# Optimization experiments

Hardware: AMD Instinct MI355X
Metric: run time of the kernel (lower is better)

Reference implementation:

```python
import jax, jax.numpy as jnp
import numpy as np
import math

N, E, D, H, EH, DEPTH = 50000, 800000, 128, 128, 16, 3
RATIO = 0.5
BN_SCALE = 1.0 / math.sqrt(1.0 + 1e-5)  # eval-mode BatchNorm1d: running mean 0, var 1
NEG_SLOPE = 0.01  # leaky_relu default


def setup_inputs() -> dict:
    key = jax.random.key(0)
    ks = jax.random.split(key, 16)
    s = lambda k, shape: jax.random.normal(k, shape, dtype=jnp.float32) * 0.05
    return {
        "x": jax.random.normal(ks[0], (N, D), dtype=jnp.float32),
        "edge_index": jax.random.randint(ks[1], (2, E), 0, N, dtype=jnp.int32),
        "edge_attr": jax.random.uniform(ks[2], (E, EH), dtype=jnp.float32),
        "We_w": s(ks[3], (EH, 1)), "We_b": s(ks[4], (1,)),
        "Wdown": s(ks[5], (DEPTH + 1, H, H)), "bdown": s(ks[6], (DEPTH + 1, H)),
        "Wpool": s(ks[7], (DEPTH, H)),
        "Wup": s(ks[8], (DEPTH, H, H)), "bup": s(ks[9], (DEPTH, H)),
        "gnorm": 1.0 + s(ks[10], (DEPTH + 1, H)), "bnorm": s(ks[11], (DEPTH + 1, H)),
        "Wr": s(ks[12], (D, D)), "br": s(ks[13], (D,)),
        "gr": 1.0 + s(ks[14], (D,)), "brn": s(ks[15], (D,)),
    }


def _bn(x, g, b):
    # eval-mode BatchNorm1d with running_mean=0, running_var=1
    return x * (g * BN_SCALE) + b


def _lrelu(x):
    return jnp.where(x > 0, x, NEG_SLOPE * x)


def _gcn(x, src, dst, w, W, b, fill):
    # PyG GCNConv: add self-loops (fill=1.0, improved -> 2.0), symmetric norm
    n = x.shape[0]
    h = x @ W  # [n, H]
    deg = jax.ops.segment_sum(w, dst, num_segments=n) + fill
    dinv = jax.lax.rsqrt(deg)
    coef = dinv[src] * w * dinv[dst]  # [E]
    agg = jax.ops.segment_sum(coef[:, None] * h[src], dst, num_segments=n)
    return agg + (fill / deg)[:, None] * h + b  # self-loop norm = fill/deg


def _topk_pool(x, src, dst, w, p, k):
    # PyG TopKPooling: score = tanh(x.p/||p||), keep top-k, scale kept x by score,
    # filter edges to kept nodes (masked edges kept at fixed length with weight 0)
    n = x.shape[0]
    score = jnp.tanh((x @ p) / jnp.linalg.norm(p))
    vals, perm = jax.lax.top_k(score, k)
    xp = x[perm] * vals[:, None]
    pos = jnp.full((n,), -1, dtype=jnp.int32).at[perm].set(jnp.arange(k, dtype=jnp.int32))
    ns, nd = pos[src], pos[dst]
    valid = (ns >= 0) & (nd >= 0)
    return (xp, jnp.where(valid, ns, 0), jnp.where(valid, nd, 0),
            jnp.where(valid, w, 0.0), perm)


def reference(x, edge_index, edge_attr, We_w, We_b, Wdown, bdown, Wpool, Wup, bup,
              gnorm, bnorm, Wr, br, gr, brn):
    src, dst = edge_index[0], edge_index[1]
    # edge embedding + min/max normalization
    ew = edge_attr @ We_w[:, 0] + We_b[0]  # [E]
    ew = ew - jnp.min(ew)
    ew = ew / (jnp.max(ew) + 1e-7)
    h = _bn(x, gnorm[0], bnorm[0])
    h = _lrelu(_gcn(h, src, dst, ew, Wdown[0], bdown[0], 1.0))
    xs, es, perms = [h], [(src, dst, ew)], []
    for i in range(DEPTH):
        k = int(math.ceil(RATIO * h.shape[0]))
        h, src, dst, ew, perm = _topk_pool(h, src, dst, ew, Wpool[i], k)
        h = _bn(h, gnorm[i + 1], bnorm[i + 1])
        h = _gcn(h, src, dst, ew, Wdown[i + 1], bdown[i + 1], 1.0)
        if i < DEPTH - 1:
            h = _lrelu(h)
            xs.append(h)
            es.append((src, dst, ew))
        perms.append(perm)
    for i in range(DEPTH):
        j = DEPTH - 1 - i
        res = xs[j]
        src, dst, ew = es[j]
        up = jnp.zeros_like(res).at[perms[j]].set(h)  # scatter unpool
        h = _gcn(res + up, src, dst, ew, Wup[i], bup[i], 2.0)  # improved=True -> fill 2
        if i < DEPTH - 1:
            h = _lrelu(h)
    g = jnp.sum(h, axis=0, keepdims=True)  # global_add_pool, single graph
    g = g @ Wr + br
    return _bn(g, gr, brn)
```

## Files before the change

kernel.cpp:

```cpp
#include <hip/hip_runtime.h>
#include <math.h>

#define N0   50000
#define E0   800000
#define HD   128
#define EHD  16
#define KP1  25000
#define KP2  12500
#define KP3  6250
#define BN_SCALE 0.9999950000374997f
#define NEG_SLOPE 0.01f
#define E1C  400000
#define E2C  120000
#define E3C  40000
#define NBE  782
#define CSB  782

#define NBIN   782
#define EPB    6144
#define NBLK   131
#define NBINP  784

typedef int   vi4 __attribute__((ext_vector_type(4)));
typedef float vf4 __attribute__((ext_vector_type(4)));
typedef __bf16 bfrag8 __attribute__((ext_vector_type(8)));
typedef float  f32x4  __attribute__((ext_vector_type(4)));

__device__ __forceinline__ unsigned fenc(float f) {
    unsigned u = __float_as_uint(f);
    return (u & 0x80000000u) ? ~u : (u | 0x80000000u);
}
__device__ __forceinline__ unsigned packbf2(float a, float b) {
    unsigned ua = __float_as_uint(a);
    unsigned ub = __float_as_uint(b);
    ua = (ua + 0x7FFFu + ((ua >> 16) & 1u)) >> 16;
    ub = (ub + 0x7FFFu + ((ub >> 16) & 1u)) >> 16;
    return ua | (ub << 16);
}
__device__ __forceinline__ void bf8_fma(float* acc, uint4 h, float c) {
    acc[0] += c * __uint_as_float(h.x << 16);
    acc[1] += c * __uint_as_float(h.x & 0xFFFF0000u);
    acc[2] += c * __uint_as_float(h.y << 16);
    acc[3] += c * __uint_as_float(h.y & 0xFFFF0000u);
    acc[4] += c * __uint_as_float(h.z << 16);
    acc[5] += c * __uint_as_float(h.z & 0xFFFF0000u);
    acc[6] += c * __uint_as_float(h.w << 16);
    acc[7] += c * __uint_as_float(h.w & 0xFFFF0000u);
}

__global__ void k_edge_ew(const float* __restrict__ ea, const float* __restrict__ Ww,
                          const float* __restrict__ Wb, float* __restrict__ ew,
                          float2* __restrict__ partials, int E) {
    int e = blockIdx.x * 256 + threadIdx.x;
    float mn = 3.4e38f, mx = -3.4e38f;
    if (e < E) {
        const float4* a4 = (const float4*)(ea + (size_t)e * EHD);
        float s = Wb[0];
        #pragma unroll
        for (int q = 0; q < 4; ++q) {
            float4 a = a4[q];
            s += a.x * Ww[q*4+0] + a.y * Ww[q*4+1] + a.z * Ww[q*4+2] + a.w * Ww[q*4+3];
        }
        ew[e] = s;
        mn = s; mx = s;
    }
    #pragma unroll
    for (int off = 32; off > 0; off >>= 1) {
        mn = fminf(mn, __shfl_xor(mn, off));
        mx = fmaxf(mx, __shfl_xor(mx, off));
    }
    __shared__ float smn[4], smx[4];
    int lane = threadIdx.x & 63, wid = threadIdx.x >> 6;
    if (lane == 0) { smn[wid] = mn; smx[wid] = mx; }
    __syncthreads();
    if (threadIdx.x == 0) {
        float a = fminf(fminf(smn[0], smn[1]), fminf(smn[2], smn[3]));
        float b = fmaxf(fmaxf(smx[0], smx[1]), fmaxf(smx[2], smx[3]));
        partials[blockIdx.x] = make_float2(a, b);
    }
}

__global__ void __launch_bounds__(1024)
k_reduce_mm(const float2* __restrict__ partials, int nb, float* __restrict__ mmv) {
    float mn = 3.4e38f, mx = -3.4e38f;
    for (int i = threadIdx.x; i < nb; i += 1024) {
        float2 t = partials[i];
        mn = fminf(mn, t.x); mx = fmaxf(mx, t.y);
    }
    #pragma unroll
    for (int off = 32; off > 0; off >>= 1) {
        mn = fminf(mn, __shfl_xor(mn, off));
        mx = fmaxf(mx, __shfl_xor(mx, off));
    }
    __shared__ float smn[16], smx[16];
    int lane = threadIdx.x & 63, wid = threadIdx.x >> 6;
    if (lane == 0) { smn[wid] = mn; smx[wid] = mx; }
    __syncthreads();
    if (threadIdx.x == 0) {
        for (int w = 1; w < 16; ++w) { mn = fminf(mn, smn[w]); mx = fmaxf(mx, smx[w]); }
        mmv[0] = mn; mmv[1] = mx;
    }
}

__global__ void __launch_bounds__(1024)
k_ew_sortA(float* __restrict__ ew, const float* __restrict__ mmv,
           const int* __restrict__ src, const int* __restrict__ dst,
           uint2* __restrict__ staging, int* __restrict__ cntM,
           int* __restrict__ locOffM, int E) {
    __shared__ uint2 sEnt[EPB];
    __shared__ int   lhist[NBINP];
    __shared__ int   sOff[NBINP];
    __shared__ int   lcur[NBINP];
    __shared__ int   wtot[16];
    int t = threadIdx.x;
    for (int i = t; i < NBINP; i += 1024) lhist[i] = 0;
    __syncthreads();
    float mn = mmv[0];
    float sc = 1.0f / ((mmv[1] - mn) + 1e-7f);
    int base = blockIdx.x * EPB;
    unsigned entx[6], enty[6];
    int bin6[6];
    #pragma unroll
    for (int it = 0; it < 6; ++it) {
        int e = base + it * 1024 + t;
        bin6[it] = -1;
        if (e < E) {
            float w = (ew[e] - mn) * sc;
            ew[e] = w;
            if (w != 0.0f) {
                int d = dst[e];
                bin6[it] = d >> 6;
                entx[it] = (unsigned)src[e] | ((unsigned)(d & 63) << 16);
                enty[it] = __float_as_uint(w);
                atomicAdd(&lhist[bin6[it]], 1);
            }
        }
    }
    __syncthreads();
    {
        int v = (t < NBINP) ? lhist[t] : 0;
        int lane = t & 63, wid = t >> 6;
        int x = v;
        #pragma unroll
        for (int off = 1; off < 64; off <<= 1) {
            int y = __shfl_up(x, off);
            if (lane >= off) x += y;
        }
        if (lane == 63) wtot[wid] = x;
        __syncthreads();
        int wb = 0;
        for (int w = 0; w < wid; ++w) wb += wtot[w];
        int excl = wb + x - v;
        if (t < NBINP) { sOff[t] = excl; lcur[t] = excl; }
    }
    __syncthreads();
    #pragma unroll
    for (int it = 0; it < 6; ++it) {
        if (bin6[it] >= 0) {
            int slot = atomicAdd(&lcur[bin6[it]], 1);
            sEnt[slot] = make_uint2(entx[it], enty[it]);
        }
    }
    __syncthreads();
    int total = sOff[NBIN];
    uint2* dstS = staging + (size_t)blockIdx.x * EPB;
    for (int i = t; i < total; i += 1024) dstS[i] = sEnt[i];
    int* cRow = cntM + blockIdx.x * NBINP;
    int* oRow = locOffM + blockIdx.x * NBINP;
    for (int i = t; i < NBINP; i += 1024) { cRow[i] = lhist[i]; oRow[i] = sOff[i]; }
}

__global__ void __launch_bounds__(1024)
k_bin_scan2(const int* __restrict__ cntM, int* __restrict__ binBase,
            int* __restrict__ rowptrEnd) {
    int t = threadIdx.x;
    int v = 0;
    if (t < NBIN) {
        for (int blk = 0; blk < NBLK; ++blk) v += cntM[blk * NBINP + t];
    }
    int lane = t & 63, wid = t >> 6;
    int xs = v;
    #pragma unroll
    for (int off = 1; off < 64; off <<= 1) {
        int y = __shfl_up(xs, off);
        if (lane >= off) xs += y;
    }
    __shared__ int wsum[16];
    if (lane == 63) wsum[wid] = xs;
    __syncthreads();
    int wb = 0;
    for (int w = 0; w < wid; ++w) wb += wsum[w];
    int excl = wb + xs - v;
    if (t < NBIN) binBase[t] = excl;
    if (t == NBIN - 1) rowptrEnd[0] = excl + v;
}

__global__ void __launch_bounds__(256)
k_binB2(const int* __restrict__ binBase, const int* __restrict__ cntM,
        const int* __restrict__ locOffM, const uint2* __restrict__ staging,
        int2* __restrict__ csr, float* __restrict__ sumW,
        int* __restrict__ rowptr, int n) {
    __shared__ uint2 raw[2048];
    __shared__ int   lhist[64];
    __shared__ int   lcur[64];
    __shared__ float lw[64];
    __shared__ int2  img[2048];
    __shared__ int   wq[4];
    __shared__ int   totalSh;
    int b = blockIdx.x;
    int t = threadIdx.x;
    int base = binBase[b];
    int c = 0, lo = 0;
    if (t < NBLK) { c = cntM[t * NBINP + b]; lo = locOffM[t * NBINP + b]; }
    int lane = t & 63, wid = t >> 6;
    int x = c;
    #pragma unroll
    for (int off = 1; off < 64; off <<= 1) {
        int y = __shfl_up(x, off);
        if (lane >= off) x += y;
    }
    if (lane == 63) wq[wid] = x;
    if (t < 64) { lhist[t] = 0; lw[t] = 0.f; }
    __syncthreads();
    int wb = 0;
    for (int w = 0; w < wid; ++w) wb += wq[w];
    int pos = wb + x - c;
    if (t == 255) totalSh = wb + x;
    __syncthreads();
    int total = min(totalSh, 2048);
    if (t < NBLK && c > 0) {
        const uint2* st = staging + (size_t)t * EPB + lo;
        for (int j = 0; j < c; ++j) {
            int p = pos + j;
            if (p < 2048) raw[p] = st[j];
        }
    }
    __syncthreads();
    for (int i = t; i < total; i += 256) {
        uint2 en = raw[i];
        int dloc = (en.x >> 16) & 63;
        atomicAdd(&lhist[dloc], 1);
        atomicAdd(&lw[dloc], __uint_as_float(en.y));
    }
    __syncthreads();
    if (t < 64) {
        int cc = lhist[t];
        int xs = cc;
        #pragma unroll
        for (int off = 1; off < 64; off <<= 1) {
            int y = __shfl_up(xs, off);
            if (t >= off) xs += y;
        }
        int excl = xs - cc;
        lcur[t] = excl;
        int v = b * 64 + t;
        if (v < n) { rowptr[v] = base + excl; sumW[v] = lw[t]; }
    }
    __syncthreads();
    for (int i = t; i < total; i += 256) {
        uint2 en = raw[i];
        int dloc = (en.x >> 16) & 63;
        int slot = atomicAdd(&lcur[dloc], 1);
        if (slot < 2048) img[slot] = make_int2((int)(en.x & 0xFFFFu), (int)en.y);
    }
    __syncthreads();
    for (int i = t; i < total; i += 256)
        csr[base + i] = img[i];
}

__global__ void __launch_bounds__(256)
k_wconv(const float* __restrict__ Wsrc, unsigned* __restrict__ WbT) {
    __shared__ ushort Wl[128][136];
    const float* W = Wsrc + (size_t)blockIdx.x * HD * HD;
    unsigned* Wo = WbT + (size_t)blockIdx.x * HD * 64;
    int tid = threadIdx.x;
    #pragma unroll
    for (int it = 0; it < 16; ++it) {
        int idx = it * 256 + tid;
        int k = idx >> 5, c4 = (idx & 31) * 4;
        float4 v = ((const float4*)(W + (size_t)k * HD))[idx & 31];
        Wl[c4 + 0][k] = (ushort)packbf2(v.x, 0.f);
        Wl[c4 + 1][k] = (ushort)packbf2(v.y, 0.f);
        Wl[c4 + 2][k] = (ushort)packbf2(v.z, 0.f);
        Wl[c4 + 3][k] = (ushort)packbf2(v.w, 0.f);
    }
    __syncthreads();
    #pragma unroll
    for (int it = 0; it < 16; ++it) {
        int idx = it * 256 + tid;
        int c = idx >> 5, j = idx & 31;
        uint2 o;
        o.x = (unsigned)Wl[c][4*j + 0] | ((unsigned)Wl[c][4*j + 1] << 16);
        o.y = (unsigned)Wl[c][4*j + 2] | ((unsigned)Wl[c][4*j + 3] << 16);
        ((uint2*)Wo)[c * 32 + j] = o;
    }
}

#define GT_ROWS 64
#define APAD 136
__global__ void __launch_bounds__(256)
k_gemm_mf(const float* __restrict__ A, const unsigned* __restrict__ WbT,
          unsigned* __restrict__ Cb, int n,
          const float* __restrict__ gs, const float* __restrict__ gb,
          const float* __restrict__ up_h, const int* __restrict__ up_pos) {
    __shared__ char ldsb[(64 + 128) * APAD * 2];
    ushort (*Al)[APAD] = (ushort(*)[APAD])ldsb;
    ushort (*Wl)[APAD] = (ushort(*)[APAD])(ldsb + 64 * APAD * 2);
    float  (*outS)[132] = (float(*)[132])ldsb;
    int tid = threadIdx.x;
    int row0 = blockIdx.x * GT_ROWS;
    int maxr = n - row0;
    #pragma unroll
    for (int it = 0; it < 8; ++it) {
        int idx = it * 256 + tid;
        int r = idx >> 5, q = idx & 31;
        float4 v = make_float4(0.f, 0.f, 0.f, 0.f);
        if (r < maxr) {
            v = ((const float4*)(A + (size_t)(row0 + r) * HD))[q];
            if (up_pos) {
                int sl = up_pos[row0 + r];
                if (sl >= 0) {
                    float4 u = ((const float4*)(up_h + (size_t)sl * HD))[q];
                    v.x += u.x; v.y += u.y; v.z += u.z; v.w += u.w;
                }
            }
            if (gs) {
                float4 g4 = ((const float4*)gs)[q];
                float4 b4 = ((const float4*)gb)[q];
                v.x = v.x * (g4.x * BN_SCALE) + b4.x;
                v.y = v.y * (g4.y * BN_SCALE) + b4.y;
                v.z = v.z * (g4.z * BN_SCALE) + b4.z;
                v.w = v.w * (g4.w * BN_SCALE) + b4.w;
            }
        }
        uint2 pk = make_uint2(packbf2(v.x, v.y), packbf2(v.z, v.w));
        *(uint2*)&Al[r][q * 4] = pk;
    }
    #pragma unroll
    for (int it = 0; it < 16; ++it) {
// ... 70 lines not shown
    #pragma unroll
    for (int off = 32; off > 0; off >>= 1) s += __shfl_down(s, off);
    if (lane == 0) ws[wid] = s;
    __syncthreads();
    if (threadIdx.x == 0) {
        __hip_atomic_store(&bsum[blockIdx.x], ws[0] + ws[1] + ws[2] + ws[3],
                           __ATOMIC_RELAXED, __HIP_MEMORY_SCOPE_AGENT);
        unsigned prev = __hip_atomic_fetch_add(dctr, 1u, __ATOMIC_ACQ_REL, __HIP_MEMORY_SCOPE_AGENT);
        lastFlag = (prev == gridDim.x - 1);
    }
    __syncthreads();
    if (!lastFlag) return;
    if (threadIdx.x < 64) {
        int nb = gridDim.x;
        int t = threadIdx.x;
        int v = (t < nb) ? __hip_atomic_load(&bsum[t], __ATOMIC_RELAXED, __HIP_MEMORY_SCOPE_AGENT) : 0;
        int x = v;
        #pragma unroll
        for (int off = 1; off < 64; off <<= 1) {
            int y = __shfl_up(x, off);
            if (t >= off) x += y;
        }
        if (t < nb) bsum[t] = x - v;
        if (t == nb - 1) totalOut[0] = x;
    }
    if (threadIdx.x == 0)
        __hip_atomic_store(dctr, 0u, __ATOMIC_RELAXED, __HIP_MEMORY_SCOPE_AGENT);
}

__global__ void k_chunk_scan(const int* __restrict__ cnt, const int* __restrict__ bo,
                             int* __restrict__ rowptr, int* __restrict__ cursor, int n) {
    __shared__ int wsum[4];
    __shared__ int running;
    int base = blockIdx.x * 1024;
    if (threadIdx.x == 0) running = bo[blockIdx.x];
    __syncthreads();
    int lane = threadIdx.x & 63, wid = threadIdx.x >> 6;
    #pragma unroll
    for (int it = 0; it < 4; ++it) {
        int i = base + it * 256 + threadIdx.x;
        int v = (i < n) ? cnt[i] : 0;
        int x = v;
        #pragma unroll
        for (int off = 1; off < 64; off <<= 1) {
            int y = __shfl_up(x, off);
            if (lane >= off) x += y;
        }
        if (lane == 63) wsum[wid] = x;
        __syncthreads();
        int wb = 0;
        for (int w = 0; w < wid; ++w) wb += wsum[w];
        int excl = running + wb + x - v;
        if (i < n) { rowptr[i] = excl; cursor[i] = excl; }
        __syncthreads();
        if (threadIdx.x == 0) running += wsum[0] + wsum[1] + wsum[2] + wsum[3];
        __syncthreads();
    }
}

__global__ void k_csr_fill(const int* __restrict__ src, const int* __restrict__ dst,
                           const float* __restrict__ w, int* __restrict__ cursor,
                           int2* __restrict__ csr,
                           const int* __restrict__ EinPtr, int EinImm) {
    int Ein = EinPtr ? EinPtr[0] : EinImm;
    int e = blockIdx.x * 256 + threadIdx.x;
    if (e >= Ein) return;
    float wv = w[e];
    if (wv == 0.0f) return;
    int slot = atomicAdd(&cursor[dst[e]], 1);
    csr[slot] = make_int2(src[e], __float_as_int(wv));
}

__global__ void k_deg_dinv(const int* __restrict__ rowptr, const int2* __restrict__ csr,
                           float fill, float* __restrict__ deg, float* __restrict__ dinv, int n) {
    int v = blockIdx.x * 256 + threadIdx.x;
    if (v >= n) return;
    float s = fill;
    int rs = rowptr[v], re = rowptr[v + 1];
    for (int j = rs; j < re; ++j) s += __int_as_float(csr[j].y);
    deg[v] = s;
    dinv[v] = rsqrtf(s);
}

__global__ void k_deg_dinv_d(const float* __restrict__ sumW, float fill,
                             float* __restrict__ deg, float* __restrict__ dinv, int n) {
    int v = blockIdx.x * 256 + threadIdx.x;
    if (v >= n) return;
    float s = fill + sumW[v];
    deg[v] = s;
    dinv[v] = rsqrtf(s);
}

__global__ void __launch_bounds__(256)
k_gcn_gather(const int* __restrict__ rowptr, const int2* __restrict__ csr,
             const float* __restrict__ deg, const float* __restrict__ dinv,
             const unsigned* __restrict__ hWb,
             const float* __restrict__ bias,
             float fill, int n, int lrelu, float* __restrict__ out) {
    int v = blockIdx.x * 4 + (threadIdx.x >> 6);
    int lane = threadIdx.x & 63;
    if (v >= n) return;
    int rs = rowptr[v], re = rowptr[v + 1];
    float dv = dinv[v];
    int quarter = lane >> 4;
    int qi = lane & 15;
    float acc[8];
    #pragma unroll
    for (int i = 0; i < 8; ++i) acc[i] = 0.f;
    for (int base = rs; base < re; base += 64) {
        int idx = base + lane;
        int s_r = 0; float c_r = 0.f;
        if (idx < re) {
            int2 ent = csr[idx];
            s_r = ent.x;
            c_r = dinv[s_r] * __int_as_float(ent.y) * dv;
        }
        int cnt = min(64, re - base);
        int groups = cnt >> 2;
        int t = 0;
        for (; t + 1 < groups; t += 2) {
            int j0 = 4 * t + quarter, j1 = j0 + 4;
            int   s0 = __shfl(s_r, j0); float c0 = __shfl(c_r, j0);
            int   s1 = __shfl(s_r, j1); float c1 = __shfl(c_r, j1);
            uint4 h0 = ((const uint4*)(hWb + (size_t)s0 * 64))[qi];
            uint4 h1 = ((const uint4*)(hWb + (size_t)s1 * 64))[qi];
            bf8_fma(acc, h0, c0);
            bf8_fma(acc, h1, c1);
        }
        for (; t < groups; ++t) {
            int j = 4 * t + quarter;
            int s = __shfl(s_r, j); float c = __shfl(c_r, j);
            uint4 h = ((const uint4*)(hWb + (size_t)s * 64))[qi];
            bf8_fma(acc, h, c);
        }
        int rem = cnt & 3;
        if (quarter < rem) {
            int j = groups * 4 + quarter;
            int s = __shfl(s_r, j); float c = __shfl(c_r, j);
            uint4 h = ((const uint4*)(hWb + (size_t)s * 64))[qi];
            bf8_fma(acc, h, c);
        }
    }
    #pragma unroll
    for (int i = 0; i < 8; ++i) {
        acc[i] += __shfl_xor(acc[i], 16);
        acc[i] += __shfl_xor(acc[i], 32);
    }
    if (quarter == 0) {
        uint4 hs = ((const uint4*)(hWb + (size_t)v * 64))[qi];
        float sc = fill / deg[v];
        float hv[8];
        hv[0] = __uint_as_float(hs.x << 16); hv[1] = __uint_as_float(hs.x & 0xFFFF0000u);
        hv[2] = __uint_as_float(hs.y << 16); hv[3] = __uint_as_float(hs.y & 0xFFFF0000u);
        hv[4] = __uint_as_float(hs.z << 16); hv[5] = __uint_as_float(hs.z & 0xFFFF0000u);
        hv[6] = __uint_as_float(hs.w << 16); hv[7] = __uint_as_float(hs.w & 0xFFFF0000u);
        float4 b0 = ((const float4*)bias)[2 * qi];
        float4 b1 = ((const float4*)bias)[2 * qi + 1];
        float o[8];
        o[0] = acc[0] + sc * hv[0] + b0.x;
        o[1] = acc[1] + sc * hv[1] + b0.y;
        o[2] = acc[2] + sc * hv[2] + b0.z;
        o[3] = acc[3] + sc * hv[3] + b0.w;
        o[4] = acc[4] + sc * hv[4] + b1.x;
        o[5] = acc[5] + sc * hv[5] + b1.y;
        o[6] = acc[6] + sc * hv[6] + b1.z;
        o[7] = acc[7] + sc * hv[7] + b1.w;
        if (lrelu) {
            #pragma unroll
            for (int i = 0; i < 8; ++i) o[i] = (o[i] > 0.f) ? o[i] : NEG_SLOPE * o[i];
        }
        float4* orow = (float4*)(out + (size_t)v * HD);
        orow[2 * qi]     = make_float4(o[0], o[1], o[2], o[3]);
        orow[2 * qi + 1] = make_float4(o[4], o[5], o[6], o[7]);
    }
}

__global__ void k_score(const float* __restrict__ x, const float* __restrict__ p,
                        float* __restrict__ score, int n, int* __restrict__ selws) {
    for (int i = blockIdx.x * 256 + threadIdx.x; i < 5120; i += gridDim.x * 256) selws[i] = 0;
    int lane = threadIdx.x & 63;
    float pv0 = p[lane], pv1 = p[lane + 64];
    float ps = pv0 * pv0 + pv1 * pv1;
    #pragma unroll
    for (int off = 32; off > 0; off >>= 1) ps += __shfl_xor(ps, off);
    float rnorm = 1.0f / sqrtf(ps);
    int node = blockIdx.x * 4 + (threadIdx.x >> 6);
    if (node >= n) return;
    const float* row = x + (size_t)node * HD;
    float s = row[lane] * pv0 + row[lane + 64] * pv1;
    #pragma unroll
    for (int off = 32; off > 0; off >>= 1) s += __shfl_xor(s, off);
    if (lane == 0) score[node] = tanhf(s * rnorm);
}

__global__ void __launch_bounds__(256)
k_histpick(const float* __restrict__ score, int n, int pass,
           unsigned* __restrict__ prefix, int* __restrict__ hist,
           int kImm, const int* __restrict__ remIn, int* __restrict__ remOut,
           unsigned* __restrict__ doneCtr) {
    __shared__ int lh[2048];
    int nbins = (pass == 2) ? 1024 : 2048;
    for (int i = threadIdx.x; i < nbins; i += 256) lh[i] = 0;
    __syncthreads();
    unsigned pfx = (pass != 0) ? prefix[0] : 0u;
    int stride = gridDim.x * 256;
    for (int i = blockIdx.x * 256 + threadIdx.x; i < n; i += stride) {
        unsigned u = fenc(score[i]);
        int bin; bool ok;
        if (pass == 0)      { bin = u >> 21;            ok = true; }
        else if (pass == 1) { bin = (u >> 10) & 2047;   ok = ((u >> 21) == (pfx >> 21)); }
        else                { bin = u & 1023;           ok = ((u >> 10) == (pfx >> 10)); }
        if (ok) atomicAdd(&lh[bin], 1);
    }
    __syncthreads();
    for (int i = threadIdx.x; i < nbins; i += 256) {
        int c = lh[i];
        if (c) __hip_atomic_fetch_add(&hist[i], c, __ATOMIC_RELAXED, __HIP_MEMORY_SCOPE_AGENT);
    }
    __syncthreads();
    __shared__ int lastFlag;
    if (threadIdx.x == 0) {
        unsigned prev = __hip_atomic_fetch_add(doneCtr, 1u, __ATOMIC_ACQ_REL, __HIP_MEMORY_SCOPE_AGENT);
        lastFlag = (prev == gridDim.x - 1);
    }
    __syncthreads();
    if (!lastFlag) return;
    __shared__ int wsum[4];
    int k = remIn ? remIn[0] : kImm;
    int t = threadIdx.x;
    int per = nbins >> 8;
    int hi = nbins - t * per, lo = hi - per;
    int s = 0;
    for (int b = lo; b < hi; ++b)
        s += __hip_atomic_load(&hist[b], __ATOMIC_RELAXED, __HIP_MEMORY_SCOPE_AGENT);
    int lane = t & 63, wid = t >> 6;
    int x = s;
    #pragma unroll
    for (int off = 1; off < 64; off <<= 1) {
        int y = __shfl_up(x, off);
        if (lane >= off) x += y;
    }
    if (lane == 63) wsum[wid] = x;
    __syncthreads();
    int wb = 0;
    for (int w = 0; w < wid; ++w) wb += wsum[w];
    int excl = wb + x - s;
    if (k > excl && k <= excl + s) {
        int cum = excl;
        int shift = (pass == 0) ? 21 : (pass == 1) ? 10 : 0;
        for (int b = hi - 1; b >= lo; --b) {
            int h = __hip_atomic_load(&hist[b], __ATOMIC_RELAXED, __HIP_MEMORY_SCOPE_AGENT);
            if (k <= cum + h) {
                unsigned base = (pass == 0) ? 0u : prefix[0];
                prefix[0] = base | ((unsigned)b << shift);
                remOut[0] = k - cum;
                break;
            }
            cum += h;
        }
    }
    __syncthreads();
    if (threadIdx.x == 0)
        __hip_atomic_store(doneCtr, 0u, __ATOMIC_RELAXED, __HIP_MEMORY_SCOPE_AGENT);
}

__global__ void k_cmp_countscan(const float* __restrict__ score, int n,
                                const unsigned* __restrict__ prefix,
                                int* __restrict__ bgt, int* __restrict__ beq,
                                unsigned* __restrict__ dctr) {
    unsigned T = prefix[0];
    int base = blockIdx.x * 1024;
    int gt = 0, eq = 0;
    #pragma unroll
    for (int it = 0; it < 4; ++it) {
        int i = base + it * 256 + threadIdx.x;
        if (i < n) {
            unsigned u = fenc(score[i]);
            gt += (u > T); eq += (u == T);
        }
    }
    __shared__ int sg[4], se[4];
    __shared__ int lastFlag;
    int lane = threadIdx.x & 63, wid = threadIdx.x >> 6;
    #pragma unroll
    for (int off = 32; off > 0; off >>= 1) { gt += __shfl_down(gt, off); eq += __shfl_down(eq, off); }
    if (lane == 0) { sg[wid] = gt; se[wid] = eq; }
    __syncthreads();
    if (threadIdx.x == 0) {
        __hip_atomic_store(&bgt[blockIdx.x], sg[0] + sg[1] + sg[2] + sg[3],
                           __ATOMIC_RELAXED, __HIP_MEMORY_SCOPE_AGENT);
        __hip_atomic_store(&beq[blockIdx.x], se[0] + se[1] + se[2] + se[3],
                           __ATOMIC_RELAXED, __HIP_MEMORY_SCOPE_AGENT);
        unsigned prev = __hip_atomic_fetch_add(dctr, 1u, __ATOMIC_ACQ_REL, __HIP_MEMORY_SCOPE_AGENT);
        lastFlag = (prev == gridDim.x - 1);
    }
    __syncthreads();
    if (!lastFlag) return;
    if (threadIdx.x < 64) {
        int nb = gridDim.x;
        int t = threadIdx.x;
        int va = (t < nb) ? __hip_atomic_load(&bgt[t], __ATOMIC_RELAXED, __HIP_MEMORY_SCOPE_AGENT) : 0;
        int vb = (t < nb) ? __hip_atomic_load(&beq[t], __ATOMIC_RELAXED, __HIP_MEMORY_SCOPE_AGENT) : 0;
        int xa = va, xb = vb;
        #pragma unroll
        for (int off = 1; off < 64; off <<= 1) {
            int ya = __shfl_up(xa, off), yb = __shfl_up(xb, off);
            if (t >= off) { xa += ya; xb += yb; }
        }
        if (t < nb) { bgt[t] = xa - va; beq[t] = xb - vb; }
    }
    if (threadIdx.x == 0)
        __hip_atomic_store(dctr, 0u, __ATOMIC_RELAXED, __HIP_MEMORY_SCOPE_AGENT);
}

__global__ void k_cmp_assign(const float* __restrict__ score, int n, int kcap,
                             const unsigned* __restrict__ prefix,
                             const int* __restrict__ selTies,
                             const int* __restrict__ bgt, const int* __restrict__ beq,
                             int* __restrict__ pos, int* __restrict__ perm,
                             float* __restrict__ vals) {
    unsigned T = prefix[0];
    int tiesNeed = selTies[0];
    __shared__ int wgt[4], weq[4];
    __shared__ int rgt, req;
    int base = blockIdx.x * 1024;
    if (threadIdx.x == 0) { rgt = bgt[blockIdx.x]; req = beq[blockIdx.x]; }
    __syncthreads();
    int lane = threadIdx.x & 63, wid = threadIdx.x >> 6;
    #pragma unroll
    for (int it = 0; it < 4; ++it) {
        int i = base + it * 256 + threadIdx.x;
        bool in = i < n;
        float sc = in ? score[i] : 0.f;
        unsigned u = in ? fenc(sc) : 0u;
        bool g = in && (u > T);
        bool e = in && (u == T);
        unsigned long long mg = __ballot(g), me = __ballot(e);
        int lgt = __popcll(mg & ((1ull << lane) - 1ull));
        int leq = __popcll(me & ((1ull << lane) - 1ull));
        if (lane == 0) { wgt[wid] = __popcll(mg); weq[wid] = __popcll(me); }
        __syncthreads();
        int wbg = 0, wbe = 0;
        for (int w = 0; w < wid; ++w) { wbg += wgt[w]; wbe += weq[w]; }
        int gtRank = rgt + wbg + lgt;
        int tieRank = req + wbe + leq;
        if (in) {
// ... 130 lines not shown

__global__ void __launch_bounds__(256)
k_colsum_part(const float* __restrict__ h, float* __restrict__ cpart, int n) {
    int c = threadIdx.x & 127;
    int rh = threadIdx.x >> 7;
    int r0 = blockIdx.x * 64;
    int r1 = min(n, r0 + 64);
    float local = 0.f;
    for (int r = r0 + rh; r < r1; r += 2) local += h[(size_t)r * HD + c];
    __shared__ float sh[256];
    sh[threadIdx.x] = local;
    __syncthreads();
    if (threadIdx.x < 128) cpart[(size_t)blockIdx.x * HD + c] = sh[c] + sh[c + 128];
}

__global__ void __launch_bounds__(1024)
k_colsum_final(const float* __restrict__ cpart, int nb,
               const float* __restrict__ Wr, const float* __restrict__ br,
               const float* __restrict__ gr, const float* __restrict__ brn,
               float* __restrict__ out) {
    __shared__ float gsh[HD];
    int c = threadIdx.x & 127;
    int seg = threadIdx.x >> 7;
    float local = 0.f;
    for (int b = seg; b < nb; b += 8) local += cpart[(size_t)b * HD + c];
    __shared__ float sh[1024];
    sh[threadIdx.x] = local;
    __syncthreads();
    if (threadIdx.x < 128) {
        float s = 0.f;
        #pragma unroll
        for (int q = 0; q < 8; ++q) s += sh[c + q * 128];
        gsh[c] = s;
    }
    __syncthreads();
    if (threadIdx.x < 128) {
        float s = br[c];
        for (int k = 0; k < HD; ++k) s += gsh[k] * Wr[k * HD + c];
        out[c] = s * (gr[c] * BN_SCALE) + brn[c];
    }
}

extern "C" void kernel_launch(void* const* d_in, const int* in_sizes, int n_in,
                              void* d_out, int out_size, void* d_ws, size_t ws_size,
                              hipStream_t stream) {
    const float* x     = (const float*)d_in[0];
    const int*   ei    = (const int*)d_in[1];
    const float* eattr = (const float*)d_in[2];
    const float* We_w  = (const float*)d_in[3];
    const float* We_b  = (const float*)d_in[4];
    const float* Wdown = (const float*)d_in[5];
    const float* bdown = (const float*)d_in[6];
    const float* Wpool = (const float*)d_in[7];
    const float* Wup   = (const float*)d_in[8];
    const float* bup   = (const float*)d_in[9];
    const float* gnorm = (const float*)d_in[10];
    const float* bnorm = (const float*)d_in[11];
    const float* Wr    = (const float*)d_in[12];
    const float* br    = (const float*)d_in[13];
    const float* gr    = (const float*)d_in[14];
    const float* brn   = (const float*)d_in[15];
    const int* src0 = ei;
    const int* dst0 = ei + E0;
    float* out = (float*)d_out;

    char* p = (char*)d_ws;
    auto alloc = [&](size_t bytes) -> void* {
        void* r = (void*)p;
        p += (bytes + 255) & ~(size_t)255;
        return r;
    };
    float* ew0  = (float*)alloc(E0 * 4);
    int* src1 = (int*)alloc(E1C * 4); int* dst1 = (int*)alloc(E1C * 4); float* ew1 = (float*)alloc(E1C * 4);
    int* src2 = (int*)alloc(E2C * 4); int* dst2 = (int*)alloc(E2C * 4); float* ew2 = (float*)alloc(E2C * 4);
    int* src3 = (int*)alloc(E3C * 4); int* dst3 = (int*)alloc(E3C * 4); float* ew3 = (float*)alloc(E3C * 4);
    float* hbuf = (float*)alloc((size_t)N0 * HD * 4);
    unsigned* hWb = (unsigned*)alloc((size_t)N0 * 64 * 4);
    float* tmp  = (float*)alloc((size_t)N0 * HD * 4);
    float* xs0  = (float*)alloc((size_t)N0 * HD * 4);
    float* xs1  = (float*)alloc((size_t)KP1 * HD * 4);
    float* xs2  = (float*)alloc((size_t)KP2 * HD * 4);
    float* deg   = (float*)alloc(N0 * 4);
    float* dinv  = (float*)alloc(N0 * 4);
    float* sumW0 = (float*)alloc(N0 * 4);
    float* score = (float*)alloc(N0 * 4);
    int*   pos1  = (int*)alloc(N0 * 4);
    int*   pos2  = (int*)alloc(N0 * 4);
    int*   pos3  = (int*)alloc(N0 * 4);
    float* vals  = (float*)alloc(KP1 * 4);
    int* perm1 = (int*)alloc(KP1 * 4);
    int* perm2 = (int*)alloc(KP2 * 4);
    int* perm3 = (int*)alloc(KP3 * 4);
    int* rowptr0 = (int*)alloc((N0 + 1) * 4);
    int* rowptr1 = (int*)alloc((KP1 + 1) * 4);
    int* rowptr2 = (int*)alloc((KP2 + 1) * 4);
    int* rowptr3 = (int*)alloc((KP3 + 1) * 4);
    int2* csrP0 = (int2*)alloc((size_t)E0 * 8);
    int2* csrP1 = (int2*)alloc((size_t)E1C * 8);
    int2* csrP2 = (int2*)alloc((size_t)E2C * 8);
    int2* csrP3 = (int2*)alloc((size_t)E3C * 8);
    int* cnt    = (int*)alloc(N0 * 4);
    int* cursor = (int*)alloc(N0 * 4);
    int* selws  = (int*)alloc(5120 * 4);
    int* hist0 = selws;
    int* hist1 = selws + 2048;
    int* hist2 = selws + 4096;
    int* bgt    = (int*)alloc(64 * 4);
    int* beq    = (int*)alloc(64 * 4);
    int* bsum   = (int*)alloc(64 * 4);
    int* bsumE  = (int*)alloc(1024 * 4);
    float2* partials = (float2*)alloc(((E0 + 255) / 256) * 8);
    float* cpart = (float*)alloc((size_t)CSB * HD * 4);
    float* mmv       = (float*)alloc(64);
    unsigned* ctrws  = (unsigned*)alloc(64 * 4);
    unsigned* dctrS  = ctrws + 0;
    unsigned* dctrH  = ctrws + 8;
    unsigned* dctrC  = ctrws + 16;
    unsigned* dctrE  = ctrws + 24;
    unsigned* prefix = (unsigned*)alloc(64);
    int* rem0        = (int*)alloc(64);
    int* rem1        = (int*)alloc(64);
    int* tiesN       = (int*)alloc(64);
    int* ecnt1       = (int*)alloc(64);
    int* ecnt2       = (int*)alloc(64);
    int* ecnt3       = (int*)alloc(64);
    int* cntM        = (int*)alloc((size_t)NBLK * NBINP * 4);
    int* locOffM     = (int*)alloc((size_t)NBLK * NBINP * 4);
    int* binBase     = (int*)alloc((NBIN + 1) * 4);
    uint2* staging   = (uint2*)tmp;
    unsigned* WbtD   = (unsigned*)alloc((size_t)7 * HD * 64 * 4);
    unsigned* WbtU   = WbtD + (size_t)4 * HD * 64;

    const int EB = (E0 + 255) / 256;

    auto build_csr = [&](const int* esrc, const int* edst, const float* eww, int n,
                         int* rowptr, int2* csrP,
                         const int* EinPtr, int EinImm, int gridE) {
        int nb = (n + 1023) / 1024;
        k_sum_scan<<<nb, 256, 0, stream>>>(cnt, bsum, n, rowptr + n, dctrS);
        k_chunk_scan<<<nb, 256, 0, stream>>>(cnt, bsum, rowptr, cursor, n);
        k_csr_fill<<<gridE, 256, 0, stream>>>(esrc, edst, eww, cursor, csrP, EinPtr, EinImm);
    };

    auto run_gcn = [&](const float* hin, const int* rowptr, const int2* csrP,
                       const float* sumW,
                       const unsigned* WbT, const float* bias, float fill, int n, int lrelu,
                       float* outbuf, const float* bn_g, const float* bn_b,
                       const float* up_h, const int* up_pos) {
        k_gemm_mf<<<(n + GT_ROWS - 1) / GT_ROWS, 256, 0, stream>>>(hin, WbT, hWb, n, bn_g, bn_b, up_h, up_pos);
        if (sumW)
            k_deg_dinv_d<<<(n + 255) / 256, 256, 0, stream>>>(sumW, fill, deg, dinv, n);
        else
            k_deg_dinv<<<(n + 255) / 256, 256, 0, stream>>>(rowptr, csrP, fill, deg, dinv, n);
        k_gcn_gather<<<(n + 3) / 4, 256, 0, stream>>>(rowptr, csrP, deg, dinv, hWb,
                                                      bias, fill, n, lrelu, outbuf);
    };

    auto run_pool = [&](const float* xin, int n, int k, const float* pvec,
                        const float* g, const float* b,
                        const int* esrc_in, const int* edst_in, const float* ew_in,
                        const int* EinPtr, int EinImm,
                        int* pos, int* perm,
                        int* esrc_out, int* edst_out, float* ew_out, int* ecntOut) {
        int nb = (n + 1023) / 1024;
        k_score<<<(n + 3) / 4, 256, 0, stream>>>(xin, pvec, score, n, selws);
        k_histpick<<<64, 256, 0, stream>>>(score, n, 0, prefix, hist0, k, (const int*)nullptr, rem0, dctrH);
        k_histpick<<<64, 256, 0, stream>>>(score, n, 1, prefix, hist1, 0, rem0, rem1, dctrH);
        k_histpick<<<64, 256, 0, stream>>>(score, n, 2, prefix, hist2, 0, rem1, tiesN, dctrH);
        k_cmp_countscan<<<nb, 256, 0, stream>>>(score, n, prefix, bgt, beq, dctrC);
        k_cmp_assign<<<nb, 256, 0, stream>>>(score, n, k, prefix, tiesN, bgt, beq, pos, perm, vals);
        k_pool_bn<<<((size_t)k * HD + 255) / 256, 256, 0, stream>>>(xin, perm, vals, g, b, hbuf, k);
        k_ecompact_countscan<<<NBE, 256, 0, stream>>>(esrc_in, edst_in, ew_in, pos, EinPtr, EinImm, k,
                                                      bsumE, ecntOut, cnt, dctrE);
        k_ecompact_assign<<<NBE, 256, 0, stream>>>(esrc_in, edst_in, ew_in, pos, EinPtr, EinImm,
                                                   bsumE, esrc_out, edst_out, ew_out, cnt);
    };

    hipMemsetAsync((void*)ctrws, 0, 64 * 4, stream);

    k_wconv<<<4, 256, 0, stream>>>(Wdown, WbtD);
    k_wconv<<<3, 256, 0, stream>>>(Wup, WbtU);

    k_edge_ew<<<EB, 256, 0, stream>>>(eattr, We_w, We_b, ew0, partials, E0);
    k_reduce_mm<<<1, 1024, 0, stream>>>(partials, EB, mmv);
    k_ew_sortA<<<NBLK, 1024, 0, stream>>>(ew0, mmv, src0, dst0, staging, cntM, locOffM, E0);

    k_bin_scan2<<<1, 1024, 0, stream>>>(cntM, binBase, rowptr0 + N0);
    k_binB2<<<NBIN, 256, 0, stream>>>(binBase, cntM, locOffM, staging, csrP0, sumW0,
                                      rowptr0, N0);

    run_gcn(x, rowptr0, csrP0, sumW0, WbtD, bdown, 1.0f, N0, 1, xs0, gnorm, bnorm, nullptr, nullptr);

    run_pool(xs0, N0, KP1, Wpool, gnorm + HD, bnorm + HD, src0, dst0, ew0,
             (const int*)nullptr, E0, pos1, perm1, src1, dst1, ew1, ecnt1);
    build_csr(src1, dst1, ew1, KP1, rowptr1, csrP1, ecnt1, 0, (E1C + 255) / 256);
    run_gcn(hbuf, rowptr1, csrP1, nullptr, WbtD + 1 * HD * 64, bdown + 1 * HD, 1.0f, KP1, 1, xs1,
            nullptr, nullptr, nullptr, nullptr);

    run_pool(xs1, KP1, KP2, Wpool + HD, gnorm + 2 * HD, bnorm + 2 * HD, src1, dst1, ew1,
             ecnt1, 0, pos2, perm2, src2, dst2, ew2, ecnt2);
    build_csr(src2, dst2, ew2, KP2, rowptr2, csrP2, ecnt2, 0, (E2C + 255) / 256);
    run_gcn(hbuf, rowptr2, csrP2, nullptr, WbtD + 2 * HD * 64, bdown + 2 * HD, 1.0f, KP2, 1, xs2,
            nullptr, nullptr, nullptr, nullptr);

    run_pool(xs2, KP2, KP3, Wpool + 2 * HD, gnorm + 3 * HD, bnorm + 3 * HD, src2, dst2, ew2,
             ecnt2, 0, pos3, perm3, src3, dst3, ew3, ecnt3);
    build_csr(src3, dst3, ew3, KP3, rowptr3, csrP3, ecnt3, 0, (E3C + 255) / 256);
    run_gcn(hbuf, rowptr3, csrP3, nullptr, WbtD + 3 * HD * 64, bdown + 3 * HD, 1.0f, KP3, 0, tmp,
            nullptr, nullptr, nullptr, nullptr);

    run_gcn(xs2, rowptr2, csrP2, nullptr, WbtU, bup, 2.0f, KP2, 1, tmp, nullptr, nullptr, tmp, pos3);

    run_gcn(xs1, rowptr1, csrP1, nullptr, WbtU + 1 * HD * 64, bup + 1 * HD, 2.0f, KP1, 1, tmp,
            nullptr, nullptr, tmp, pos2);

    run_gcn(xs0, rowptr0, csrP0, sumW0, WbtU + 2 * HD * 64, bup + 2 * HD, 2.0f, N0, 0, tmp,
            nullptr, nullptr, tmp, pos1);

    k_colsum_part<<<CSB, 256, 0, stream>>>(tmp, cpart, N0);
    k_colsum_final<<<1, 1024, 0, stream>>>(cpart, CSB, Wr, br, gr, brn, out);
}
```

Baseline: 720.8 us.

## Merge small kernels via last-block reductions, grid flags, and precomputed degrees

```diff
diff --git a/kernel.cpp b/kernel.cpp
--- a/kernel.cpp
+++ b/kernel.cpp
@@ -47,10 +47,18 @@
     acc[6] += c * __uint_as_float(h.w << 16);
     acc[7] += c * __uint_as_float(h.w & 0xFFFF0000u);
 }
+__device__ __forceinline__ void spin_flag(unsigned* f) {
+    if (threadIdx.x == 0) {
+        while (__hip_atomic_load(f, __ATOMIC_ACQUIRE, __HIP_MEMORY_SCOPE_AGENT) == 0u)
+            __builtin_amdgcn_s_sleep(8);
+    }
+    __syncthreads();
+}
 
 __global__ void k_edge_ew(const float* __restrict__ ea, const float* __restrict__ Ww,
                           const float* __restrict__ Wb, float* __restrict__ ew,
-                          float2* __restrict__ partials, int E) {
+                          float2* __restrict__ partials, float* __restrict__ mmv,
+                          unsigned* __restrict__ dctr, int E) {
     int e = blockIdx.x * 256 + threadIdx.x;
     float mn = 3.4e38f, mx = -3.4e38f;
     if (e < E) {
@@ -70,6 +78,7 @@
         mx = fmaxf(mx, __shfl_xor(mx, off));
     }
     __shared__ float smn[4], smx[4];
+    __shared__ int lastFlag;
     int lane = threadIdx.x & 63, wid = threadIdx.x >> 6;
     if (lane == 0) { smn[wid] = mn; smx[wid] = mx; }
     __syncthreads();
@@ -77,28 +86,29 @@
         float a = fminf(fminf(smn[0], smn[1]), fminf(smn[2], smn[3]));
         float b = fmaxf(fmaxf(smx[0], smx[1]), fmaxf(smx[2], smx[3]));
         partials[blockIdx.x] = make_float2(a, b);
-    }
-}
-
-__global__ void __launch_bounds__(1024)
-k_reduce_mm(const float2* __restrict__ partials, int nb, float* __restrict__ mmv) {
-    float mn = 3.4e38f, mx = -3.4e38f;
-    for (int i = threadIdx.x; i < nb; i += 1024) {
+        unsigned prev = __hip_atomic_fetch_add(dctr, 1u, __ATOMIC_ACQ_REL, __HIP_MEMORY_SCOPE_AGENT);
+        lastFlag = (prev == gridDim.x - 1);
+    }
+    __syncthreads();
+    if (!lastFlag) return;
+    float fmn = 3.4e38f, fmx = -3.4e38f;
+    for (int i = threadIdx.x; i < gridDim.x; i += 256) {
         float2 t = partials[i];
-        mn = fminf(mn, t.x); mx = fmaxf(mx, t.y);
+        fmn = fminf(fmn, t.x); fmx = fmaxf(fmx, t.y);
     }
     #pragma unroll
     for (int off = 32; off > 0; off >>= 1) {
-        mn = fminf(mn, __shfl_xor(mn, off));
-        mx = fmaxf(mx, __shfl_xor(mx, off));
-    }
-    __shared__ float smn[16], smx[16];
-    int lane = threadIdx.x & 63, wid = threadIdx.x >> 6;
-    if (lane == 0) { smn[wid] = mn; smx[wid] = mx; }
+        fmn = fminf(fmn, __shfl_xor(fmn, off));
+        fmx = fmaxf(fmx, __shfl_xor(fmx, off));
+    }
+    __syncthreads();
+    if (lane == 0) { smn[wid] = fmn; smx[wid] = fmx; }
     __syncthreads();
     if (threadIdx.x == 0) {
-        for (int w = 1; w < 16; ++w) { mn = fminf(mn, smn[w]); mx = fmaxf(mx, smx[w]); }
-        mmv[0] = mn; mmv[1] = mx;
+        float a = fminf(fminf(smn[0], smn[1]), fminf(smn[2], smn[3]));
+        float b = fmaxf(fmaxf(smx[0], smx[1]), fmaxf(smx[2], smx[3]));
+        mmv[0] = a; mmv[1] = b;
+        __hip_atomic_store(dctr, 0u, __ATOMIC_RELAXED, __HIP_MEMORY_SCOPE_AGENT);
     }
 }
 
@@ -198,7 +208,9 @@
 __global__ void __launch_bounds__(256)
 k_binB2(const int* __restrict__ binBase, const int* __restrict__ cntM,
         const int* __restrict__ locOffM, const uint2* __restrict__ staging,
-        int2* __restrict__ csr, float* __restrict__ sumW,
+        int2* __restrict__ csr,
+        float* __restrict__ deg1, float* __restrict__ dinv1,
+        float* __restrict__ deg2, float* __restrict__ dinv2,
         int* __restrict__ rowptr, int n) {
     __shared__ uint2 raw[2048];
     __shared__ int   lhist[64];
@@ -254,7 +266,13 @@
         int excl = xs - cc;
         lcur[t] = excl;
         int v = b * 64 + t;
-        if (v < n) { rowptr[v] = base + excl; sumW[v] = lw[t]; }
+        if (v < n) {
+            rowptr[v] = base + excl;
+            float s1 = 1.0f + lw[t];
+            float s2 = 2.0f + lw[t];
+            deg1[v] = s1; dinv1[v] = rsqrtf(s1);
+            deg2[v] = s2; dinv2[v] = rsqrtf(s2);
+        }
     }
     __syncthreads();
     for (int i = t; i < total; i += 256) {
@@ -491,15 +509,6 @@
     dinv[v] = rsqrtf(s);
 }
 
-__global__ void k_deg_dinv_d(const float* __restrict__ sumW, float fill,
-                             float* __restrict__ deg, float* __restrict__ dinv, int n) {
-    int v = blockIdx.x * 256 + threadIdx.x;
-    if (v >= n) return;
-    float s = fill + sumW[v];
-    deg[v] = s;
-    dinv[v] = rsqrtf(s);
-}
-
 __global__ void __launch_bounds__(256)
 k_gcn_gather(const int* __restrict__ rowptr, const int2* __restrict__ csr,
              const float* __restrict__ deg, const float* __restrict__ dinv,
@@ -527,14 +536,20 @@
         int cnt = min(64, re - base);
         int groups = cnt >> 2;
         int t = 0;
-        for (; t + 1 < groups; t += 2) {
-            int j0 = 4 * t + quarter, j1 = j0 + 4;
+        for (; t + 3 < groups; t += 4) {
+            int j0 = 4 * t + quarter, j1 = j0 + 4, j2 = j0 + 8, j3 = j0 + 12;
             int   s0 = __shfl(s_r, j0); float c0 = __shfl(c_r, j0);
             int   s1 = __shfl(s_r, j1); float c1 = __shfl(c_r, j1);
+            int   s2 = __shfl(s_r, j2); float c2 = __shfl(c_r, j2);
+            int   s3 = __shfl(s_r, j3); float c3 = __shfl(c_r, j3);
             uint4 h0 = ((const uint4*)(hWb + (size_t)s0 * 64))[qi];
             uint4 h1 = ((const uint4*)(hWb + (size_t)s1 * 64))[qi];
+            uint4 h2 = ((const uint4*)(hWb + (size_t)s2 * 64))[qi];
+            uint4 h3 = ((const uint4*)(hWb + (size_t)s3 * 64))[qi];
             bf8_fma(acc, h0, c0);
             bf8_fma(acc, h1, c1);
+            bf8_fma(acc, h2, c2);
+            bf8_fma(acc, h3, c3);
         }
         for (; t < groups; ++t) {
             int j = 4 * t + quarter;
@@ -603,74 +618,99 @@
 }
 
 __global__ void __launch_bounds__(256)
-k_histpick(const float* __restrict__ score, int n, int pass,
-           unsigned* __restrict__ prefix, int* __restrict__ hist,
-           int kImm, const int* __restrict__ remIn, int* __restrict__ remOut,
-           unsigned* __restrict__ doneCtr) {
+k_histpick3(const float* __restrict__ score, int n, int kSel,
+            unsigned* __restrict__ prefix,
+            int* __restrict__ hist0, int* __restrict__ hist1, int* __restrict__ hist2,
+            int* __restrict__ rem0, int* __restrict__ rem1, int* __restrict__ tiesN,
+            unsigned* __restrict__ dc0, unsigned* __restrict__ dc1, unsigned* __restrict__ dc2,
+            unsigned* __restrict__ flag0, unsigned* __restrict__ flag1) {
     __shared__ int lh[2048];
-    int nbins = (pass == 2) ? 1024 : 2048;
-    for (int i = threadIdx.x; i < nbins; i += 256) lh[i] = 0;
-    __syncthreads();
-    unsigned pfx = (pass != 0) ? prefix[0] : 0u;
+    __shared__ int wsum[4];
+    __shared__ int lastFlag;
     int stride = gridDim.x * 256;
-    for (int i = blockIdx.x * 256 + threadIdx.x; i < n; i += stride) {
-        unsigned u = fenc(score[i]);
-        int bin; bool ok;
-        if (pass == 0)      { bin = u >> 21;            ok = true; }
-        else if (pass == 1) { bin = (u >> 10) & 2047;   ok = ((u >> 21) == (pfx >> 21)); }
-        else                { bin = u & 1023;           ok = ((u >> 10) == (pfx >> 10)); }
-        if (ok) atomicAdd(&lh[bin], 1);
-    }
-    __syncthreads();
-    for (int i = threadIdx.x; i < nbins; i += 256) {
-        int c = lh[i];
-        if (c) __hip_atomic_fetch_add(&hist[i], c, __ATOMIC_RELAXED, __HIP_MEMORY_SCOPE_AGENT);
-    }
-    __syncthreads();
-    __shared__ int lastFlag;
-    if (threadIdx.x == 0) {
-        unsigned prev = __hip_atomic_fetch_add(doneCtr, 1u, __ATOMIC_ACQ_REL, __HIP_MEMORY_SCOPE_AGENT);
-        lastFlag = (prev == gridDim.x - 1);
-    }
-    __syncthreads();
-    if (!lastFlag) return;
-    __shared__ int wsum[4];
-    int k = remIn ? remIn[0] : kImm;
-    int t = threadIdx.x;
-    int per = nbins >> 8;
-    int hi = nbins - t * per, lo = hi - per;
-    int s = 0;
-    for (int b = lo; b < hi; ++b)
-        s += __hip_atomic_load(&hist[b], __ATOMIC_RELAXED, __HIP_MEMORY_SCOPE_AGENT);
-    int lane = t & 63, wid = t >> 6;
-    int x = s;
-    #pragma unroll
-    for (int off = 1; off < 64; off <<= 1) {
-        int y = __shfl_up(x, off);
-        if (lane >= off) x += y;
-    }
-    if (lane == 63) wsum[wid] = x;
-    __syncthreads();
-    int wb = 0;
-    for (int w = 0; w < wid; ++w) wb += wsum[w];
-    int excl = wb + x - s;
-    if (k > excl && k <= excl + s) {
-        int cum = excl;
-        int shift = (pass == 0) ? 21 : (pass == 1) ? 10 : 0;
-        for (int b = hi - 1; b >= lo; --b) {
-            int h = __hip_atomic_load(&hist[b], __ATOMIC_RELAXED, __HIP_MEMORY_SCOPE_AGENT);
-            if (k <= cum + h) {
-                unsigned base = (pass == 0) ? 0u : prefix[0];
-                prefix[0] = base | ((unsigned)b << shift);
-                remOut[0] = k - cum;
-                break;
+    unsigned pfx = 0;
+    int kRem = kSel;
+    #pragma unroll 1
+    for (int pass = 0; pass < 3; ++pass) {
+        int nbins = (pass == 2) ? 1024 : 2048;
+        int* hist = (pass == 0) ? hist0 : (pass == 1) ? hist1 : hist2;
+        unsigned* dctr = (pass == 0) ? dc0 : (pass == 1) ? dc1 : dc2;
+        for (int i = threadIdx.x; i < nbins; i += 256) lh[i] = 0;
+        __syncthreads();
+        for (int i = blockIdx.x * 256 + threadIdx.x; i < n; i += stride) {
+            unsigned u = fenc(score[i]);
+            int bin; bool ok;
+            if (pass == 0)      { bin = u >> 21;          ok = true; }
+            else if (pass == 1) { bin = (u >> 10) & 2047; ok = ((u >> 21) == (pfx >> 21)); }
+            else                { bin = u & 1023;         ok = ((u >> 10) == (pfx >> 10)); }
+            if (ok) atomicAdd(&lh[bin], 1);
+        }
+        __syncthreads();
+        for (int i = threadIdx.x; i < nbins; i += 256) {
+            int c = lh[i];
+            if (c) __hip_atomic_fetch_add(&hist[i], c, __ATOMIC_RELAXED, __HIP_MEMORY_SCOPE_AGENT);
+        }
+        __syncthreads();
+        if (threadIdx.x == 0) {
+            unsigned prev = __hip_atomic_fetch_add(dctr, 1u, __ATOMIC_ACQ_REL, __HIP_MEMORY_SCOPE_AGENT);
+            lastFlag = (prev == gridDim.x - 1);
+        }
+        __syncthreads();
+        if (lastFlag) {
+            int t = threadIdx.x;
+            int per = nbins >> 8;
+            int hi = nbins - t * per, lo2 = hi - per;
+            int s = 0;
+            for (int b = lo2; b < hi; ++b)
+                s += __hip_atomic_load(&hist[b], __ATOMIC_RELAXED, __HIP_MEMORY_SCOPE_AGENT);
+            int lane = t & 63, wid = t >> 6;
+            int x = s;
+            #pragma unroll
+            for (int off = 1; off < 64; off <<= 1) {
+                int y = __shfl_up(x, off);
+                if (lane >= off) x += y;
             }
-            cum += h;
-        }
-    }
-    __syncthreads();
-    if (threadIdx.x == 0)
-        __hip_atomic_store(doneCtr, 0u, __ATOMIC_RELAXED, __HIP_MEMORY_SCOPE_AGENT);
+            if (lane == 63) wsum[wid] = x;
+            __syncthreads();
+            int wb = 0;
+            for (int w = 0; w < wid; ++w) wb += wsum[w];
+            int excl = wb + x - s;
+            if (kRem > excl && kRem <= excl + s) {
+                int cum = excl;
+                int shift = (pass == 0) ? 21 : (pass == 1) ? 10 : 0;
+                for (int b = hi - 1; b >= lo2; --b) {
+                    int h = __hip_atomic_load(&hist[b], __ATOMIC_RELAXED, __HIP_MEMORY_SCOPE_AGENT);
+                    if (kRem <= cum + h) {
+                        unsigned np = ((pass == 0) ? 0u : pfx) | ((unsigned)b << shift);
+                        __hip_atomic_store(prefix, np, __ATOMIC_RELAXED, __HIP_MEMORY_SCOPE_AGENT);
+                        int* remP = (pass == 0) ? rem0 : (pass == 1) ? rem1 : tiesN;
+                        __hip_atomic_store(remP, kRem - cum, __ATOMIC_RELAXED, __HIP_MEMORY_SCOPE_AGENT);
+                        break;
+                    }
+                    cum += h;
+                }
+            }
+            __syncthreads();
+            if (threadIdx.x == 0) {
+                __hip_atomic_store(dctr, 0u, __ATOMIC_RELAXED, __HIP_MEMORY_SCOPE_AGENT);
+                if (pass == 0)
+                    __hip_atomic_store(flag0, 1u, __ATOMIC_RELEASE, __HIP_MEMORY_SCOPE_AGENT);
+                else if (pass == 1)
+                    __hip_atomic_store(flag1, 1u, __ATOMIC_RELEASE, __HIP_MEMORY_SCOPE_AGENT);
+                else {
+                    __hip_atomic_store(flag0, 0u, __ATOMIC_RELAXED, __HIP_MEMORY_SCOPE_AGENT);
+                    __hip_atomic_store(flag1, 0u, __ATOMIC_RELAXED, __HIP_MEMORY_SCOPE_AGENT);
+                }
+            }
+        }
+        if (pass < 2) {
+            spin_flag((pass == 0) ? flag0 : flag1);
+            pfx = __hip_atomic_load(prefix, __ATOMIC_RELAXED, __HIP_MEMORY_SCOPE_AGENT);
+            kRem = __hip_atomic_load((pass == 0) ? rem0 : rem1,
+                                     __ATOMIC_RELAXED, __HIP_MEMORY_SCOPE_AGENT);
+            __syncthreads();
+        }
+    }
 }
 
 __global__ void k_cmp_countscan(const float* __restrict__ score, int n,
@@ -967,7 +1007,10 @@
     float* xs2  = (float*)alloc((size_t)KP2 * HD * 4);
     float* deg   = (float*)alloc(N0 * 4);
     float* dinv  = (float*)alloc(N0 * 4);
-    float* sumW0 = (float*)alloc(N0 * 4);
+    float* deg1  = (float*)alloc(N0 * 4);
+    float* dinv1 = (float*)alloc(N0 * 4);
+    float* deg2  = (float*)alloc(N0 * 4);
+    float* dinv2 = (float*)alloc(N0 * 4);
     float* score = (float*)alloc(N0 * 4);
     int*   pos1  = (int*)alloc(N0 * 4);
     int*   pos2  = (int*)alloc(N0 * 4);
@@ -999,9 +1042,14 @@
     float* mmv       = (float*)alloc(64);
     unsigned* ctrws  = (unsigned*)alloc(64 * 4);
     unsigned* dctrS  = ctrws + 0;
-    unsigned* dctrH  = ctrws + 8;
-    unsigned* dctrC  = ctrws + 16;
-    unsigned* dctrE  = ctrws + 24;
+    unsigned* dctrC  = ctrws + 8;
+    unsigned* dctrE  = ctrws + 16;
+    unsigned* dctrM  = ctrws + 24;
+    unsigned* dcP0   = ctrws + 32;
+    unsigned* dcP1   = ctrws + 40;
+    unsigned* dcP2   = ctrws + 48;
+    unsigned* flag0  = ctrws + 56;
+    unsigned* flag1  = ctrws + 60;
     unsigned* prefix = (unsigned*)alloc(64);
     int* rem0        = (int*)alloc(64);
     int* rem1        = (int*)alloc(64);
@@ -1028,16 +1076,15 @@
     };
 
     auto run_gcn = [&](const float* hin, const int* rowptr, const int2* csrP,
-                       const float* sumW,
+                       const float* degP, const float* dinvP, bool degFromCsr,
                        const unsigned* WbT, const float* bias, float fill, int n, int lrelu,
                        float* outbuf, const float* bn_g, const float* bn_b,
                        const float* up_h, const int* up_pos) {
         k_gemm_mf<<<(n + GT_ROWS - 1) / GT_ROWS, 256, 0, stream>>>(hin, WbT, hWb, n, bn_g, bn_b, up_h, up_pos);
-        if (sumW)
-            k_deg_dinv_d<<<(n + 255) / 256, 256, 0, stream>>>(sumW, fill, deg, dinv, n);
-        else
-            k_deg_dinv<<<(n + 255) / 256, 256, 0, stream>>>(rowptr, csrP, fill, deg, dinv, n);
-        k_gcn_gather<<<(n + 3) / 4, 256, 0, stream>>>(rowptr, csrP, deg, dinv, hWb,
+        if (degFromCsr)
+            k_deg_dinv<<<(n + 255) / 256, 256, 0, stream>>>(rowptr, csrP, fill,
+                                                            (float*)degP, (float*)dinvP, n);
+        k_gcn_gather<<<(n + 3) / 4, 256, 0, stream>>>(rowptr, csrP, degP, dinvP, hWb,
                                                       bias, fill, n, lrelu, outbuf);
     };
 
@@ -1049,9 +1096,8 @@
                         int* esrc_out, int* edst_out, float* ew_out, int* ecntOut) {
         int nb = (n + 1023) / 1024;
         k_score<<<(n + 3) / 4, 256, 0, stream>>>(xin, pvec, score, n, selws);
-        k_histpick<<<64, 256, 0, stream>>>(score, n, 0, prefix, hist0, k, (const int*)nullptr, rem0, dctrH);
-        k_histpick<<<64, 256, 0, stream>>>(score, n, 1, prefix, hist1, 0, rem0, rem1, dctrH);
-        k_histpick<<<64, 256, 0, stream>>>(score, n, 2, prefix, hist2, 0, rem1, tiesN, dctrH);
+        k_histpick3<<<64, 256, 0, stream>>>(score, n, k, prefix, hist0, hist1, hist2,
+                                            rem0, rem1, tiesN, dcP0, dcP1, dcP2, flag0, flag1);
         k_cmp_countscan<<<nb, 256, 0, stream>>>(score, n, prefix, bgt, beq, dctrC);
         k_cmp_assign<<<nb, 256, 0, stream>>>(score, n, k, prefix, tiesN, bgt, beq, pos, perm, vals);
         k_pool_bn<<<((size_t)k * HD + 255) / 256, 256, 0, stream>>>(xin, perm, vals, g, b, hbuf, k);
@@ -1066,41 +1112,42 @@
     k_wconv<<<4, 256, 0, stream>>>(Wdown, WbtD);
     k_wconv<<<3, 256, 0, stream>>>(Wup, WbtU);
 
-    k_edge_ew<<<EB, 256, 0, stream>>>(eattr, We_w, We_b, ew0, partials, E0);
-    k_reduce_mm<<<1, 1024, 0, stream>>>(partials, EB, mmv);
+    k_edge_ew<<<EB, 256, 0, stream>>>(eattr, We_w, We_b, ew0, partials, mmv, dctrM, E0);
     k_ew_sortA<<<NBLK, 1024, 0, stream>>>(ew0, mmv, src0, dst0, staging, cntM, locOffM, E0);
 
     k_bin_scan2<<<1, 1024, 0, stream>>>(cntM, binBase, rowptr0 + N0);
-    k_binB2<<<NBIN, 256, 0, stream>>>(binBase, cntM, locOffM, staging, csrP0, sumW0,
-                                      rowptr0, N0);
-
-    run_gcn(x, rowptr0, csrP0, sumW0, WbtD, bdown, 1.0f, N0, 1, xs0, gnorm, bnorm, nullptr, nullptr);
+    k_binB2<<<NBIN, 256, 0, stream>>>(binBase, cntM, locOffM, staging, csrP0,
+                                      deg1, dinv1, deg2, dinv2, rowptr0, N0);
+
+    run_gcn(x, rowptr0, csrP0, deg1, dinv1, false, WbtD, bdown, 1.0f, N0, 1, xs0,
+            gnorm, bnorm, nullptr, nullptr);
 
     run_pool(xs0, N0, KP1, Wpool, gnorm + HD, bnorm + HD, src0, dst0, ew0,
              (const int*)nullptr, E0, pos1, perm1, src1, dst1, ew1, ecnt1);
     build_csr(src1, dst1, ew1, KP1, rowptr1, csrP1, ecnt1, 0, (E1C + 255) / 256);
-    run_gcn(hbuf, rowptr1, csrP1, nullptr, WbtD + 1 * HD * 64, bdown + 1 * HD, 1.0f, KP1, 1, xs1,
-            nullptr, nullptr, nullptr, nullptr);
+    run_gcn(hbuf, rowptr1, csrP1, deg, dinv, true, WbtD + 1 * HD * 64, bdown + 1 * HD,
+            1.0f, KP1, 1, xs1, nullptr, nullptr, nullptr, nullptr);
 
     run_pool(xs1, KP1, KP2, Wpool + HD, gnorm + 2 * HD, bnorm + 2 * HD, src1, dst1, ew1,
              ecnt1, 0, pos2, perm2, src2, dst2, ew2, ecnt2);
     build_csr(src2, dst2, ew2, KP2, rowptr2, csrP2, ecnt2, 0, (E2C + 255) / 256);
-    run_gcn(hbuf, rowptr2, csrP2, nullptr, WbtD + 2 * HD * 64, bdown + 2 * HD, 1.0f, KP2, 1, xs2,
-            nullptr, nullptr, nullptr, nullptr);
+    run_gcn(hbuf, rowptr2, csrP2, deg, dinv, true, WbtD + 2 * HD * 64, bdown + 2 * HD,
+            1.0f, KP2, 1, xs2, nullptr, nullptr, nullptr, nullptr);
 
     run_pool(xs2, KP2, KP3, Wpool + 2 * HD, gnorm + 3 * HD, bnorm + 3 * HD, src2, dst2, ew2,
              ecnt2, 0, pos3, perm3, src3, dst3, ew3, ecnt3);
     build_csr(src3, dst3, ew3, KP3, rowptr3, csrP3, ecnt3, 0, (E3C + 255) / 256);
-    run_gcn(hbuf, rowptr3, csrP3, nullptr, WbtD + 3 * HD * 64, bdown + 3 * HD, 1.0f, KP3, 0, tmp,
-            nullptr, nullptr, nullptr, nullptr);
-
-    run_gcn(xs2, rowptr2, csrP2, nullptr, WbtU, bup, 2.0f, KP2, 1, tmp, nullptr, nullptr, tmp, pos3);
-
-    run_gcn(xs1, rowptr1, csrP1, nullptr, WbtU + 1 * HD * 64, bup + 1 * HD, 2.0f, KP1, 1, tmp,
-            nullptr, nullptr, tmp, pos2);
-
-    run_gcn(xs0, rowptr0, csrP0, sumW0, WbtU + 2 * HD * 64, bup + 2 * HD, 2.0f, N0, 0, tmp,
-            nullptr, nullptr, tmp, pos1);
+    run_gcn(hbuf, rowptr3, csrP3, deg, dinv, true, WbtD + 3 * HD * 64, bdown + 3 * HD,
+            1.0f, KP3, 0, tmp, nullptr, nullptr, nullptr, nullptr);
+
+    run_gcn(xs2, rowptr2, csrP2, deg, dinv, true, WbtU, bup, 2.0f, KP2, 1, tmp,
+            nullptr, nullptr, tmp, pos3);
+
+    run_gcn(xs1, rowptr1, csrP1, deg, dinv, true, WbtU + 1 * HD * 64, bup + 1 * HD,
+            2.0f, KP1, 1, tmp, nullptr, nullptr, tmp, pos2);
+
+    run_gcn(xs0, rowptr0, csrP0, deg2, dinv2, false, WbtU + 2 * HD * 64, bup + 2 * HD,
+            2.0f, N0, 0, tmp, nullptr, nullptr, tmp, pos1);
 
     k_colsum_part<<<CSB, 256, 0, stream>>>(tmp, cpart, N0);
     k_colsum_final<<<1, 1024, 0, stream>>>(cpart, CSB, Wr, br, gr, brn, out);
```

Measured after the change: 859.0 us. 1.19x slower.
